# Kernel optimization log

Measured on AMD Instinct MI355X. Metric: run time of the kernel, lower is better.

Reference implementation:

```python
import jax, jax.numpy as jnp
import numpy as np

NUM_CLASSES = 80
IMG = 608.0
L_COORD, L_NOOBJ, L_CLS = 5.0, 0.5, 1.0
EPS = 1e-7
ANCHORS = jnp.array([[12,16],[19,36],[40,28],[36,75],[76,55],[72,146],
                     [142,110],[192,243],[459,401]], dtype=jnp.float32).reshape(3, 3, 2)


def _iou(b1, b2):
    # boxes in (cx, cy, w, h); broadcastable shapes [..., 4]
    b1x1 = b1[..., 0] - b1[..., 2] * 0.5; b1y1 = b1[..., 1] - b1[..., 3] * 0.5
    b1x2 = b1[..., 0] + b1[..., 2] * 0.5; b1y2 = b1[..., 1] + b1[..., 3] * 0.5
    b2x1 = b2[..., 0] - b2[..., 2] * 0.5; b2y1 = b2[..., 1] - b2[..., 3] * 0.5
    b2x2 = b2[..., 0] + b2[..., 2] * 0.5; b2y2 = b2[..., 1] + b2[..., 3] * 0.5
    iw = jnp.clip(jnp.minimum(b1x2, b2x2) - jnp.maximum(b1x1, b2x1), 0.0)
    ih = jnp.clip(jnp.minimum(b1y2, b2y2) - jnp.maximum(b1y1, b2y1), 0.0)
    inter = iw * ih
    union = (b1x2 - b1x1) * (b1y2 - b1y1) + (b2x2 - b2x1) * (b2y2 - b2y1) - inter + EPS
    return inter / union


def _scale_loss(pred, anchors, targets):
    # pred: [B, A, H, W, 5+C]; anchors: [A, 2] (pixels); targets: [B, T, 5+C]
    B, A, H, W, _ = pred.shape
    C = pred.shape[-1] - 5
    T = targets.shape[1]

    # ---- decode predictions (decodePredictionsStable) ----
    gy, gx = jnp.meshgrid(jnp.arange(H), jnp.arange(W), indexing='ij')
    grid = jnp.stack([gx, gy], axis=-1).astype(pred.dtype)          # [H, W, 2]
    xy = jax.nn.sigmoid(pred[..., :2])
    wh = jnp.clip(pred[..., 2:4], -10.0, 10.0)
    box_xy = jnp.clip((xy + grid) / jnp.array([W, H], dtype=pred.dtype), 0.0, 1.0)
    box_wh = jnp.clip(jnp.exp(wh) * anchors[None, :, None, None, :] / IMG, 0.0, 1.0)
    pbox = jnp.concatenate([box_xy, box_wh], axis=-1)               # [B,A,H,W,4]
    pconf = jax.nn.sigmoid(pred[..., 4])                            # [B,A,H,W]
    pcls = jax.nn.sigmoid(pred[..., 5:])                            # [B,A,H,W,C]

    # ---- build targets (buildTargetsStable, vectorized scatter) ----
    gtbox = jnp.clip(targets[..., :4], 0.0, 1.0)                    # [B,T,4]
    valid = targets[..., 4] > 0                                     # [B,T]
    gxi = jnp.clip((gtbox[..., 0] * W).astype(jnp.int32), 0, W - 1)
    gyi = jnp.clip((gtbox[..., 1] * H).astype(jnp.int32), 0, H - 1)
    abox = jnp.concatenate([jnp.full((A, 2), 0.5, dtype=pred.dtype), anchors / IMG], axis=-1)
    ious = _iou(abox[None, None, :, :], gtbox[:, :, None, :])       # [B,T,A]
    best = jnp.argmax(ious, axis=-1).astype(jnp.int32)              # first max == torch strict '>' loop
    bidx = jnp.broadcast_to(jnp.arange(B, dtype=jnp.int32)[:, None], (B, T))

    flat = ((bidx * A + best) * H + gyi) * W + gxi                  # [B,T]
    order = jnp.arange(B * T, dtype=jnp.int32).reshape(B, T)
    ncells = B * A * H * W
    winner = jnp.full((ncells,), -1, jnp.int32).at[jnp.where(valid, flat, ncells)].max(order, mode='drop')
    keep = valid & (winner[flat] == order)
    bw = jnp.where(keep, bidx, B)                                   # out-of-range -> dropped

    mask = jnp.zeros((B, A, H, W), pred.dtype).at[bw, best, gyi, gxi].set(1.0, mode='drop')
    tbox = jnp.zeros((B, A, H, W, 4), pred.dtype).at[bw, best, gyi, gxi].set(gtbox, mode='drop')
    tcls = jnp.zeros((B, A, H, W, C), pred.dtype).at[bw, best, gyi, gxi].set(targets[..., 5:5 + C], mode='drop')

    npos = jnp.sum(mask)
    nneg = jnp.asarray(mask.size, pred.dtype) - npos

    # ---- coordinate loss: mean(1 - IoU) over positives ----
    coord = jnp.where(npos > 0, jnp.sum((1.0 - _iou(pbox, tbox)) * mask) / jnp.maximum(npos, 1.0), 0.0)

    # ---- confidence loss: BCE sum/npos + lambdaNoObj * BCE sum/nneg ----
    p = jnp.clip(pconf, 1e-10, 1.0 - 1e-10)
    bce = -(mask * jnp.log(p) + (1.0 - mask) * jnp.log1p(-p))
    conf = jnp.sum(bce * mask) / jnp.maximum(npos, 1.0) \
         + L_NOOBJ * jnp.sum(bce * (1.0 - mask)) / jnp.maximum(nneg, 1.0)

    # ---- class loss: BCE mean over positive rows ----
    pc = jnp.clip(pcls, 1e-10, 1.0 - 1e-10)
    tc = jnp.clip(tcls, 0.0, 1.0)
    bcec = -(tc * jnp.log(pc) + (1.0 - tc) * jnp.log1p(-pc))
    cls = jnp.where(npos > 0, jnp.sum(bcec * mask[..., None]) / jnp.maximum(npos * C, 1.0), 0.0)

    return coord, conf, cls


def setup_inputs() -> dict:
    key = jax.random.key(0)
    k0, k1, k2, k3 = jax.random.split(key, 4)
    B, T, C = 16, 50, NUM_CLASSES
    pred0 = jax.random.normal(k0, (B, 3, 76, 76, 5 + C), dtype=jnp.float32)
    pred1 = jax.random.normal(k1, (B, 3, 38, 38, 5 + C), dtype=jnp.float32)
    pred2 = jax.random.normal(k2, (B, 3, 19, 19, 5 + C), dtype=jnp.float32)
    targets = jax.random.uniform(k3, (B, T, 5 + C), dtype=jnp.float32)
    return {"pred0": pred0, "pred1": pred1, "pred2": pred2, "targets": targets}


def reference(pred0, pred1, pred2, targets):
    coord = jnp.float32(0.0); conf = jnp.float32(0.0); cls = jnp.float32(0.0)
    for s, pred in enumerate((pred0, pred1, pred2)):
        c, cf, cl = _scale_loss(pred, ANCHORS[s], targets)
        coord = coord + c; conf = conf + cf; cls = cls + cl
    total = L_COORD * coord + conf + L_CLS * cls
    return total, coord, conf, cls
```

## Files before the change

kernel.cpp:

```cpp
#include <hip/hip_runtime.h>
#include <math.h>

#define BB   16
#define TT   50
#define BT   (BB*TT)
#define NCLS 80
#define IMGF 608.0f

#define H0 76
#define H1 38
#define H2 19
#define N0 277248
#define N1 69312
#define N2 17328
#define NTOT (N0+N1+N2)

#define CELLS_PER_THREAD 8
#define NBLK ((NTOT + 256*CELLS_PER_THREAD - 1) / (256*CELLS_PER_THREAD))
#define NWAVE (NBLK * 4)
#define NPOS  (3 * BT)

__constant__ float c_anchors[3][3][2] = {
    {{12.f,16.f},{19.f,36.f},{40.f,28.f}},
    {{36.f,75.f},{76.f,55.f},{72.f,146.f}},
    {{142.f,110.f},{192.f,243.f},{459.f,401.f}}};
__constant__ int c_H[3] = {H0, H1, H2};

__device__ __forceinline__ float sigmoidf_(float x) { return 1.0f / (1.0f + expf(-x)); }
__device__ __forceinline__ float clipf_(float x, float lo, float hi) {
    return fminf(fmaxf(x, lo), hi);
}

__device__ __forceinline__ float iou4(float ax, float ay, float aw, float ah,
                                      float bx, float by, float bw, float bh) {
    float ax1 = ax - aw * 0.5f, ay1 = ay - ah * 0.5f;
    float ax2 = ax + aw * 0.5f, ay2 = ay + ah * 0.5f;
    float bx1 = bx - bw * 0.5f, by1 = by - bh * 0.5f;
    float bx2 = bx + bw * 0.5f, by2 = by + bh * 0.5f;
    float iw = fmaxf(fminf(ax2, bx2) - fmaxf(ax1, bx1), 0.f);
    float ih = fmaxf(fminf(ay2, by2) - fmaxf(ay1, by1), 0.f);
    float inter = iw * ih;
    float uni = (ax2 - ax1) * (ay2 - ay1) + (bx2 - bx1) * (by2 - by1) - inter + 1e-7f;
    return inter / uni;
}

__device__ __forceinline__ int target_cell(const float* tr, int s, float& cx, float& cy,
                                           float& w, float& h, int& best, int& gxi, int& gyi) {
    float t4 = tr[4];
    if (!(t4 > 0.f)) return -1;
    cx = clipf_(tr[0], 0.f, 1.f);
    cy = clipf_(tr[1], 0.f, 1.f);
    w  = clipf_(tr[2], 0.f, 1.f);
    h  = clipf_(tr[3], 0.f, 1.f);
    best = 0;
    float bi = -1e30f;
    #pragma unroll
    for (int a = 0; a < 3; a++) {
        float aw = c_anchors[s][a][0] / IMGF;
        float ah = c_anchors[s][a][1] / IMGF;
        float v = iou4(0.5f, 0.5f, aw, ah, cx, cy, w, h);
        if (v > bi) { bi = v; best = a; }
    }
    int H = c_H[s];
    gxi = (int)(cx * (float)H); gxi = min(max(gxi, 0), H - 1);
    gyi = (int)(cy * (float)H); gyi = min(max(gyi, 0), H - 1);
    return 0;
}

__global__ __launch_bounds__(256) void k_main(const float* __restrict__ p0,
                                              const float* __restrict__ p1,
                                              const float* __restrict__ p2,
                                              const float* __restrict__ targets,
                                              float* __restrict__ noobj_part,
                                              float* __restrict__ pos_part) {
    int blk = blockIdx.x;
    int lane = threadIdx.x & 63;
    int wv = threadIdx.x >> 6;

    int base = blk * (256 * CELLS_PER_THREAD) + threadIdx.x;
    float vals[CELLS_PER_THREAD];
    #pragma unroll
    for (int k = 0; k < CELLS_PER_THREAD; k++) {
        int g = base + k * 256;
        const float* pred; int c;
        if (g < N0)            { pred = p0; c = g; }
        else if (g < N0 + N1)  { pred = p1; c = g - N0; }
        else                   { pred = p2; c = g - N0 - N1; }
        vals[k] = (g < NTOT) ? pred[(long long)c * 85 + 4] : 0.f;
    }
    float sum[3] = {0.f, 0.f, 0.f};
    #pragma unroll
    for (int k = 0; k < CELLS_PER_THREAD; k++) {
        int g = base + k * 256;
        if (g < NTOT) {
            float p = clipf_(sigmoidf_(vals[k]), 1e-10f, 1.0f);
            float v = -log1pf(-p);
            if (g < N0)           sum[0] += v;
            else if (g < N0 + N1) sum[1] += v;
            else                  sum[2] += v;
        }
    }
    #pragma unroll
    for (int off = 32; off > 0; off >>= 1) {
        sum[0] += __shfl_xor(sum[0], off, 64);
        sum[1] += __shfl_xor(sum[1], off, 64);
        sum[2] += __shfl_xor(sum[2], off, 64);
    }
    __shared__ float sm[4][3];
    if (lane == 0) { sm[wv][0] = sum[0]; sm[wv][1] = sum[1]; sm[wv][2] = sum[2]; }
    __syncthreads();
    if (threadIdx.x < 3)
        noobj_part[blk * 3 + threadIdx.x] =
            sm[0][threadIdx.x] + sm[1][threadIdx.x] + sm[2][threadIdx.x] + sm[3][threadIdx.x];

    int gw = blk * 4 + wv;
    for (int item = gw; item < NPOS; item += NWAVE) {
        int s = item / BT;
        int order = item % BT;
        int b = order / TT, t = order % TT;

        float v_coord = 0.f, v_obj = 0.f, v_noadj = 0.f, v_cls = 0.f, v_np = 0.f;

        const float* tr = targets + order * 85;
        float cx, cy, w, h; int best, gxi, gyi;
        if (target_cell(tr, s, cx, cy, w, h, best, gxi, gyi) == 0) {
            int H = c_H[s];
            int flat = ((b * 3 + best) * H + gyi) * H + gxi;

            bool lost = false;
            int tp = t + 1 + lane;
            if (tp < TT) {
                const float* tr2 = targets + (b * TT + tp) * 85;
                float cx2, cy2, w2, h2; int best2, gxi2, gyi2;
                if (target_cell(tr2, s, cx2, cy2, w2, h2, best2, gxi2, gyi2) == 0) {
                    int flat2 = ((b * 3 + best2) * H + gyi2) * H + gxi2;
                    lost = (flat2 == flat);
                }
            }
            if (__ballot(lost) == 0ull) {
                const float* pred = (s == 0) ? p0 : (s == 1) ? p1 : p2;
                const float* pc = pred + (long long)flat * 85;

                float px = sigmoidf_(pc[0]);
                float py = sigmoidf_(pc[1]);
                float bx = clipf_((px + (float)gxi) / (float)H, 0.f, 1.f);
                float by = clipf_((py + (float)gyi) / (float)H, 0.f, 1.f);
                float aw = c_anchors[s][best][0], ah = c_anchors[s][best][1];
                float bwv = clipf_(expf(clipf_(pc[2], -10.f, 10.f)) * aw / IMGF, 0.f, 1.f);
                float bhv = clipf_(expf(clipf_(pc[3], -10.f, 10.f)) * ah / IMGF, 0.f, 1.f);
                float iou = iou4(bx, by, bwv, bhv, cx, cy, w, h);

                float p = clipf_(sigmoidf_(pc[4]), 1e-10f, 1.0f);

                float pcv = clipf_(sigmoidf_(pc[5 + lane]), 1e-10f, 1.0f);
                float tc  = clipf_(tr[5 + lane], 0.f, 1.f);
                float cl  = -(tc * logf(pcv) + (1.f - tc) * log1pf(-pcv));
                if (lane < NCLS - 64) {
                    float pcv2 = clipf_(sigmoidf_(pc[5 + 64 + lane]), 1e-10f, 1.0f);
                    float tc2  = clipf_(tr[5 + 64 + lane], 0.f, 1.f);
                    cl += -(tc2 * logf(pcv2) + (1.f - tc2) * log1pf(-pcv2));
                }
                #pragma unroll
                for (int off = 32; off > 0; off >>= 1) cl += __shfl_xor(cl, off, 64);

                v_coord = 1.f - iou;
                v_obj   = -logf(p);
                v_noadj = -log1pf(-p);
                v_cls   = cl;
                v_np    = 1.f;
            }
        }

        if (lane == 0) {
            float* dst = pos_part + (long long)item * 5;
            dst[0] = v_coord; dst[1] = v_obj; dst[2] = v_noadj;
            dst[3] = v_cls;   dst[4] = v_np;
        }
    }
}

__global__ __launch_bounds__(256) void k_final(const float* __restrict__ noobj_part,
                                               const float* __restrict__ pos_part,
                                               float* __restrict__ out) {
    float nsum[3] = {0.f, 0.f, 0.f};
    for (int i = threadIdx.x; i < NBLK; i += 256) {
        #pragma unroll
        for (int s = 0; s < 3; s++) nsum[s] += noobj_part[i * 3 + s];
    }
    float ps[3][5] = {};
    for (int i = threadIdx.x; i < NPOS; i += 256) {
        int s = i / BT;
        #pragma unroll
        for (int q = 0; q < 5; q++) ps[s][q] += pos_part[i * 5 + q];
    }

    __shared__ float red[18][256];
    #pragma unroll
    for (int s = 0; s < 3; s++) {
        red[s][threadIdx.x] = nsum[s];
        #pragma unroll
        for (int q = 0; q < 5; q++) red[3 + s * 5 + q][threadIdx.x] = ps[s][q];
    }
    __syncthreads();
    for (int off = 128; off > 0; off >>= 1) {
        if (threadIdx.x < off) {
            #pragma unroll
            for (int r = 0; r < 18; r++)
                red[r][threadIdx.x] += red[r][threadIdx.x + off];
        }
        __syncthreads();
    }
    if (threadIdx.x == 0) {
        const float ncell[3] = {(float)N0, (float)N1, (float)N2};
        float coord = 0.f, conf = 0.f, cls = 0.f;
        #pragma unroll
        for (int s = 0; s < 3; s++) {
            float noobjTot = red[s][0];
            float co    = red[3 + s * 5 + 0][0];
            float ob    = red[3 + s * 5 + 1][0];
            float noadj = red[3 + s * 5 + 2][0];
            float cl    = red[3 + s * 5 + 3][0];
            float npos  = red[3 + s * 5 + 4][0];
            float nneg = ncell[s] - npos;
            float dn = fmaxf(npos, 1.f);
            conf += ob / dn + 0.5f * (noobjTot - noadj) / fmaxf(nneg, 1.f);
            if (npos > 0.f) {
                coord += co / dn;
                cls   += cl / fmaxf(npos * (float)NCLS, 1.f);
            }
        }
        out[0] = 5.0f * coord + conf + 1.0f * cls;
        out[1] = coord;
        out[2] = conf;
        out[3] = cls;
    }
}

extern "C" void kernel_launch(void* const* d_in, const int* in_sizes, int n_in,
                              void* d_out, int out_size, void* d_ws, size_t ws_size,
                              hipStream_t stream) {
    const float* p0 = (const float*)d_in[0];
    const float* p1 = (const float*)d_in[1];
    const float* p2 = (const float*)d_in[2];
    const float* tg = (const float*)d_in[3];
    float* out = (float*)d_out;

    char* ws = (char*)d_ws;
    float* noobj_part = (float*)ws;
    float* pos_part   = (float*)(ws + 4096);

    k_main<<<NBLK, 256, 0, stream>>>(p0, p1, p2, tg, noobj_part, pos_part);
    k_final<<<1, 256, 0, stream>>>(noobj_part, pos_part, out);
}
```

Baseline: 173.3 us.

## Stream full prediction tensors with coalesced float4 loads and split positive-target blocks

Replaces the strided per-cell load of the objectness logit (one float every 85 floats) with fully coalesced float4 streaming over the whole prediction tensors. Each thread tests whether its vector contains an index-4 element and accumulates the no-object BCE term. Work is split into dedicated streaming blocks per scale and separate blocks that each handle four positive-target items, so those items are no longer interleaved with the streaming work. This reads roughly all of the prediction data instead of one element per cache line, trading more DRAM traffic and a modulo per vector for perfectly coalesced access.

```diff
diff --git a/kernel.cpp b/kernel.cpp
--- a/kernel.cpp
+++ b/kernel.cpp
@@ -15,10 +15,18 @@
 #define N2 17328
 #define NTOT (N0+N1+N2)
 
-#define CELLS_PER_THREAD 8
-#define NBLK ((NTOT + 256*CELLS_PER_THREAD - 1) / (256*CELLS_PER_THREAD))
-#define NWAVE (NBLK * 4)
-#define NPOS  (3 * BT)
+#define F0 5891520
+#define F1 1472880
+#define F2 368220
+
+#define SB0 1600
+#define SB1 400
+#define SB2 100
+#define NSTREAM (SB0+SB1+SB2)
+
+#define NPOS (3*BT)
+#define NPOSBLK (NPOS/4)
+#define NBLK (NPOSBLK + NSTREAM)
 
 __constant__ float c_anchors[3][3][2] = {
     {{12.f,16.f},{19.f,36.f},{40.f,28.f}},
@@ -77,44 +85,34 @@
     int lane = threadIdx.x & 63;
     int wv = threadIdx.x >> 6;
 
-    int base = blk * (256 * CELLS_PER_THREAD) + threadIdx.x;
-    float vals[CELLS_PER_THREAD];
-    #pragma unroll
-    for (int k = 0; k < CELLS_PER_THREAD; k++) {
-        int g = base + k * 256;
-        const float* pred; int c;
-        if (g < N0)            { pred = p0; c = g; }
-        else if (g < N0 + N1)  { pred = p1; c = g - N0; }
-        else                   { pred = p2; c = g - N0 - N1; }
-        vals[k] = (g < NTOT) ? pred[(long long)c * 85 + 4] : 0.f;
-    }
-    float sum[3] = {0.f, 0.f, 0.f};
-    #pragma unroll
-    for (int k = 0; k < CELLS_PER_THREAD; k++) {
-        int g = base + k * 256;
-        if (g < NTOT) {
-            float p = clipf_(sigmoidf_(vals[k]), 1e-10f, 1.0f);
-            float v = -log1pf(-p);
-            if (g < N0)           sum[0] += v;
-            else if (g < N0 + N1) sum[1] += v;
-            else                  sum[2] += v;
-        }
-    }
-    #pragma unroll
-    for (int off = 32; off > 0; off >>= 1) {
-        sum[0] += __shfl_xor(sum[0], off, 64);
-        sum[1] += __shfl_xor(sum[1], off, 64);
-        sum[2] += __shfl_xor(sum[2], off, 64);
-    }
-    __shared__ float sm[4][3];
-    if (lane == 0) { sm[wv][0] = sum[0]; sm[wv][1] = sum[1]; sm[wv][2] = sum[2]; }
-    __syncthreads();
-    if (threadIdx.x < 3)
-        noobj_part[blk * 3 + threadIdx.x] =
-            sm[0][threadIdx.x] + sm[1][threadIdx.x] + sm[2][threadIdx.x] + sm[3][threadIdx.x];
-
-    int gw = blk * 4 + wv;
-    for (int item = gw; item < NPOS; item += NWAVE) {
+    if (blk >= NPOSBLK) {
+        int sblk = blk - NPOSBLK;
+        const float4* p4; unsigned nf4; int local, nb;
+        if (sblk < SB0)            { p4 = (const float4*)p0; nf4 = F0; local = sblk;            nb = SB0; }
+        else if (sblk < SB0 + SB1) { p4 = (const float4*)p1; nf4 = F1; local = sblk - SB0;      nb = SB1; }
+        else                       { p4 = (const float4*)p2; nf4 = F2; local = sblk - SB0 - SB1; nb = SB2; }
+
+        float acc = 0.f;
+        unsigned stride = (unsigned)nb * 256u;
+        for (unsigned i = (unsigned)local * 256u + threadIdx.x; i < nf4; i += stride) {
+            float4 v = p4[i];
+            unsigned r = (i * 4u) % 85u;
+            if (r >= 1u && r <= 4u) {
+                unsigned k = 4u - r;
+                float lg = (k == 0u) ? v.x : (k == 1u) ? v.y : (k == 2u) ? v.z : v.w;
+                float p = clipf_(sigmoidf_(lg), 1e-10f, 1.0f);
+                acc += -log1pf(-p);
+            }
+        }
+        #pragma unroll
+        for (int off = 32; off > 0; off >>= 1) acc += __shfl_xor(acc, off, 64);
+        __shared__ float sm[4];
+        if (lane == 0) sm[wv] = acc;
+        __syncthreads();
+        if (threadIdx.x == 0)
+            noobj_part[sblk] = sm[0] + sm[1] + sm[2] + sm[3];
+    } else {
+        int item = blk * 4 + wv;
         int s = item / BT;
         int order = item % BT;
         int b = order / TT, t = order % TT;
@@ -183,9 +181,11 @@
                                                const float* __restrict__ pos_part,
                                                float* __restrict__ out) {
     float nsum[3] = {0.f, 0.f, 0.f};
-    for (int i = threadIdx.x; i < NBLK; i += 256) {
-        #pragma unroll
-        for (int s = 0; s < 3; s++) nsum[s] += noobj_part[i * 3 + s];
+    for (int i = threadIdx.x; i < NSTREAM; i += 256) {
+        float v = noobj_part[i];
+        if (i < SB0)            nsum[0] += v;
+        else if (i < SB0 + SB1) nsum[1] += v;
+        else                    nsum[2] += v;
     }
     float ps[3][5] = {};
     for (int i = threadIdx.x; i < NPOS; i += 256) {
@@ -247,7 +247,7 @@
 
     char* ws = (char*)d_ws;
     float* noobj_part = (float*)ws;
-    float* pos_part   = (float*)(ws + 4096);
+    float* pos_part   = (float*)(ws + 16384);
 
     k_main<<<NBLK, 256, 0, stream>>>(p0, p1, p2, tg, noobj_part, pos_part);
     k_final<<<1, 256, 0, stream>>>(noobj_part, pos_part, out);
```

After: 179.2 us. 1.03x slower.
